# Performance work log

Hardware: AMD Instinct MI355X
Metric: run time of the kernel (lower is better)

The kernel has to match this reference:

```python
import jax, jax.numpy as jnp
import numpy as np


def setup_inputs() -> dict:
    key = jax.random.key(0)
    kx, kq, kb, kc = jax.random.split(key, 4)
    N, D = 16384, 1024
    x = jax.random.normal(kx, (N, D), dtype=jnp.float32)
    Q = jax.random.normal(kq, (D, D), dtype=jnp.float32)
    b = jax.random.normal(kb, (D,), dtype=jnp.float32)
    c = jax.random.normal(kc, (1,), dtype=jnp.float32)
    return {"x": x, "Q": Q, "b": b, "c": c}


def reference(x, Q, b, c):
    # y_i = x_i^T Q x_i + b^T x_i + c  (same math as diag(x @ Q @ x.T)
    # without materializing the NxN matrix)
    xQ = x @ Q                                # [N, D]
    quad = jnp.sum(xQ * x, axis=-1)           # [N]
    y = quad + x @ b + c                       # [N] (c broadcasts from [1])
    return y[:, None]                          # [N, 1]
```

## Files before the change

kernel.cpp:

```cpp
#include <hip/hip_runtime.h>
#include <hip/hip_bf16.h>


#define DD 1024
#define KH 256
#define KSTEP 8
#define NROUND 16
#define LDS_ROW 264

typedef short v8s __attribute__((ext_vector_type(8)));
typedef float v4f __attribute__((ext_vector_type(4)));

__device__ __forceinline__ short f2b(float f) {
    union { __hip_bfloat16 h; short s; } u;
    u.h = __float2bfloat16(f);
    return u.s;
}

__global__ __launch_bounds__(512, 2)
void quad_kernel(const float* __restrict__ x, const float* __restrict__ Q,
                 const float* __restrict__ bvec, const float* __restrict__ cptr,
                 float* __restrict__ y)
{
    __shared__ short lq[2][32 * LDS_ROW];

    const int tid  = threadIdx.x;
    const int lane = tid & 63;
    const int wave = tid >> 6;
    const int quad = lane >> 4;
    const int l15  = lane & 15;

    const int seg  = blockIdx.x & 7;
    const int rblk = blockIdx.x >> 3;
    const int kq   = seg >> 1;
    const int cs   = seg & 1;

    const int row_base = rblk * 256 + wave * 32;
    const int kofs     = kq * KH;
    const int col_base = cs * 512;

    v8s a[2][KSTEP];
    #pragma unroll
    for (int g = 0; g < 2; ++g) {
        const float* xr = x + (size_t)(row_base + g * 16 + l15) * DD + kofs + quad * 8;
        #pragma unroll
        for (int s = 0; s < KSTEP; ++s) {
            const float4 f0 = *(const float4*)(xr + s * 32);
            const float4 f1 = *(const float4*)(xr + s * 32 + 4);
            v8s t;
            t[0]=f2b(f0.x); t[1]=f2b(f0.y); t[2]=f2b(f0.z); t[3]=f2b(f0.w);
            t[4]=f2b(f1.x); t[5]=f2b(f1.y); t[6]=f2b(f1.z); t[7]=f2b(f1.w);
            a[g][s] = t;
            asm volatile("" : "+a"(a[g][s]));
        }
    }

    int s_nn[4], s_k4[4];
    #pragma unroll
    for (int i = 0; i < 4; ++i) {
        const int idx = tid + i * 512;
        s_nn[i] = idx >> 6;
        s_k4[i] = idx & 63;
    }

    float4 pf[4];
    #pragma unroll
    for (int i = 0; i < 4; ++i)
        pf[i] = *(const float4*)(Q + (size_t)(col_base + s_nn[i]) * DD + kofs + s_k4[i] * 4);

    float acc[2][4];
    #pragma unroll
    for (int g = 0; g < 2; ++g)
        #pragma unroll
        for (int r = 0; r < 4; ++r) acc[g][r] = 0.f;

    for (int t = 0; t < NROUND; ++t) {
        short* dst = &lq[t & 1][0];
        #pragma unroll
        for (int i = 0; i < 4; ++i) {
            const float4 f = pf[i];
            short4 s;
            s.x=f2b(f.x); s.y=f2b(f.y); s.z=f2b(f.z); s.w=f2b(f.w);
            *(short4*)&dst[s_nn[i] * LDS_ROW + s_k4[i] * 4] = s;
        }
        __syncthreads();

        if (t + 1 < NROUND) {
            #pragma unroll
            for (int i = 0; i < 4; ++i)
                pf[i] = *(const float4*)(Q + (size_t)(col_base + (t + 1) * 32 + s_nn[i]) * DD + kofs + s_k4[i] * 4);
        }

        const int n0 = col_base + t * 32 + l15;
        const float bn0 = (kq == 0) ? bvec[n0]      : 0.f;
        const float bn1 = (kq == 0) ? bvec[n0 + 16] : 0.f;
        float xv[2][2][4];
        {
            const float* xc = x + (size_t)(row_base + quad * 4) * DD + n0;
            #pragma unroll
            for (int nt = 0; nt < 2; ++nt)
                #pragma unroll
                for (int g = 0; g < 2; ++g)
                    #pragma unroll
                    for (int r = 0; r < 4; ++r)
                        xv[nt][g][r] = xc[(size_t)(g * 16 + r) * DD + nt * 16];
        }

        v4f cf[2][2];
        #pragma unroll
        for (int nt = 0; nt < 2; ++nt)
            #pragma unroll
            for (int g = 0; g < 2; ++g) cf[nt][g] = (v4f){0.f, 0.f, 0.f, 0.f};
        const short* bp = &lq[t & 1][l15 * LDS_ROW + quad * 8];
        #pragma unroll
        for (int s = 0; s < KSTEP; ++s) {
            const v8s b0 = *(const v8s*)(bp + s * 32);
            const v8s b1 = *(const v8s*)(bp + 16 * LDS_ROW + s * 32);
            #pragma unroll
            for (int g = 0; g < 2; ++g) {
                cf[0][g] = __builtin_amdgcn_mfma_f32_16x16x32_bf16(a[g][s], b0, cf[0][g], 0, 0, 0);
                cf[1][g] = __builtin_amdgcn_mfma_f32_16x16x32_bf16(a[g][s], b1, cf[1][g], 0, 0, 0);
            }
        }

        #pragma unroll
        for (int g = 0; g < 2; ++g)
            #pragma unroll
            for (int r = 0; r < 4; ++r)
                acc[g][r] += (cf[0][g][r] + bn0) * xv[0][g][r]
                           + (cf[1][g][r] + bn1) * xv[1][g][r];
    }

    const float cc = (seg == 0) ? cptr[0] : 0.f;
    #pragma unroll
    for (int g = 0; g < 2; ++g) {
        #pragma unroll
        for (int r = 0; r < 4; ++r) {
            float v = acc[g][r];
            v += __shfl_xor(v, 1); v += __shfl_xor(v, 2);
            v += __shfl_xor(v, 4); v += __shfl_xor(v, 8);
            if (l15 == 0)
                atomicAdd(&y[row_base + g * 16 + quad * 4 + r], v + cc);
        }
    }
}

extern "C" void kernel_launch(void* const* d_in, const int* in_sizes, int n_in,
                              void* d_out, int out_size, void* d_ws, size_t ws_size,
                              hipStream_t stream)
{
    const float* x = (const float*)d_in[0];
    const float* Q = (const float*)d_in[1];
    const float* b = (const float*)d_in[2];
    const float* c = (const float*)d_in[3];
    float* y = (float*)d_out;

    hipMemsetAsync(y, 0, (size_t)out_size * sizeof(float), stream);
    quad_kernel<<<dim3(512), dim3(512), 0, stream>>>(x, Q, b, c, y);
}
```

Baseline: 152.4 us.

## Stream Q tiles via global_load_lds with swizzled fp32 LDS and smaller K split

```diff
diff --git a/kernel.cpp b/kernel.cpp
--- a/kernel.cpp
+++ b/kernel.cpp
@@ -3,10 +3,11 @@
 
 
 #define DD 1024
-#define KH 256
-#define KSTEP 8
-#define NROUND 16
-#define LDS_ROW 264
+#define KH 128
+#define KSTEP 4
+#define NT 64
+#define ROWB 512
+#define TILEB 8192
 
 typedef short v8s __attribute__((ext_vector_type(8)));
 typedef float v4f __attribute__((ext_vector_type(4)));
@@ -17,12 +18,12 @@
     return u.s;
 }
 
-__global__ __launch_bounds__(512, 2)
+__global__ __launch_bounds__(256, 4)
 void quad_kernel(const float* __restrict__ x, const float* __restrict__ Q,
                  const float* __restrict__ bvec, const float* __restrict__ cptr,
                  float* __restrict__ y)
 {
-    __shared__ short lq[2][32 * LDS_ROW];
+    __shared__ __align__(1024) float lq[2][16 * KH];
 
     const int tid  = threadIdx.x;
     const int lane = tid & 63;
@@ -30,14 +31,28 @@
     const int quad = lane >> 4;
     const int l15  = lane & 15;
 
-    const int seg  = blockIdx.x & 7;
+    const int kq   = blockIdx.x & 7;
     const int rblk = blockIdx.x >> 3;
-    const int kq   = seg >> 1;
-    const int cs   = seg & 1;
+    const int row_base = rblk * 128 + wave * 32;
+    const int kofs = kq * KH;
 
-    const int row_base = rblk * 256 + wave * 32;
-    const int kofs     = kq * KH;
-    const int col_base = cs * 512;
+    int grow[2], goff[2];
+    #pragma unroll
+    for (int j = 0; j < 2; ++j) {
+        const int r = wave * 4 + j * 2 + (lane >> 5);
+        grow[j] = r;
+        goff[j] = ((lane & 31) * 16) ^ ((r & 7) << 4);
+    }
+
+    #pragma unroll
+    for (int j = 0; j < 2; ++j) {
+        const char* gp = (const char*)(Q + (size_t)grow[j] * DD + kofs) + goff[j];
+        __builtin_amdgcn_global_load_lds(
+            (const __attribute__((address_space(1))) unsigned int*)gp,
+            (__attribute__((address_space(3))) unsigned int*)
+                ((char*)&lq[0][0] + (wave * 4 + j * 2) * ROWB),
+            16, 0, 0);
+    }
 
     v8s a[2][KSTEP];
     #pragma unroll
@@ -55,18 +70,10 @@
         }
     }
 
-    int s_nn[4], s_k4[4];
-    #pragma unroll
-    for (int i = 0; i < 4; ++i) {
-        const int idx = tid + i * 512;
-        s_nn[i] = idx >> 6;
-        s_k4[i] = idx & 63;
-    }
-
-    float4 pf[4];
-    #pragma unroll
-    for (int i = 0; i < 4; ++i)
-        pf[i] = *(const float4*)(Q + (size_t)(col_base + s_nn[i]) * DD + kofs + s_k4[i] * 4);
+    const int xorc = (l15 & 7) << 4;
+    const int lp0 = l15 * ROWB + ((quad * 32     ) ^ xorc);
+    const int lp1 = l15 * ROWB + ((quad * 32 + 16) ^ xorc);
+    const char* lbase = (const char*)&lq[0][0];
 
     float acc[2][4];
     #pragma unroll
@@ -74,64 +81,56 @@
         #pragma unroll
         for (int r = 0; r < 4; ++r) acc[g][r] = 0.f;
 
-    for (int t = 0; t < NROUND; ++t) {
-        short* dst = &lq[t & 1][0];
-        #pragma unroll
-        for (int i = 0; i < 4; ++i) {
-            const float4 f = pf[i];
-            short4 s;
-            s.x=f2b(f.x); s.y=f2b(f.y); s.z=f2b(f.z); s.w=f2b(f.w);
-            *(short4*)&dst[s_nn[i] * LDS_ROW + s_k4[i] * 4] = s;
-        }
+    for (int t = 0; t < NT; ++t) {
         __syncthreads();
 
-        if (t + 1 < NROUND) {
+        if (t + 1 < NT) {
             #pragma unroll
-            for (int i = 0; i < 4; ++i)
-                pf[i] = *(const float4*)(Q + (size_t)(col_base + (t + 1) * 32 + s_nn[i]) * DD + kofs + s_k4[i] * 4);
+            for (int j = 0; j < 2; ++j) {
+                const char* gp = (const char*)(Q + (size_t)((t + 1) * 16 + grow[j]) * DD + kofs) + goff[j];
+                __builtin_amdgcn_global_load_lds(
+                    (const __attribute__((address_space(1))) unsigned int*)gp,
+                    (__attribute__((address_space(3))) unsigned int*)
+                        ((char*)&lq[(t + 1) & 1][0] + (wave * 4 + j * 2) * ROWB),
+                    16, 0, 0);
+            }
         }
 
-        const int n0 = col_base + t * 32 + l15;
-        const float bn0 = (kq == 0) ? bvec[n0]      : 0.f;
-        const float bn1 = (kq == 0) ? bvec[n0 + 16] : 0.f;
-        float xv[2][2][4];
+        const int n0 = t * 16 + l15;
+        const float bn = (kq == 0) ? bvec[n0] : 0.f;
+        float xv[2][4];
         {
             const float* xc = x + (size_t)(row_base + quad * 4) * DD + n0;
             #pragma unroll
-            for (int nt = 0; nt < 2; ++nt)
+            for (int g = 0; g < 2; ++g)
                 #pragma unroll
-                for (int g = 0; g < 2; ++g)
-                    #pragma unroll
-                    for (int r = 0; r < 4; ++r)
-                        xv[nt][g][r] = xc[(size_t)(g * 16 + r) * DD + nt * 16];
+                for (int r = 0; r < 4; ++r)
+                    xv[g][r] = xc[(size_t)(g * 16 + r) * DD];
         }
 
-        v4f cf[2][2];
-        #pragma unroll
-        for (int nt = 0; nt < 2; ++nt)
-            #pragma unroll
-            for (int g = 0; g < 2; ++g) cf[nt][g] = (v4f){0.f, 0.f, 0.f, 0.f};
-        const short* bp = &lq[t & 1][l15 * LDS_ROW + quad * 8];
+        const char* lb = lbase + (t & 1) * TILEB;
+        v4f cf[2];
+        cf[0] = (v4f){0.f, 0.f, 0.f, 0.f};
+        cf[1] = (v4f){0.f, 0.f, 0.f, 0.f};
         #pragma unroll
         for (int s = 0; s < KSTEP; ++s) {
-            const v8s b0 = *(const v8s*)(bp + s * 32);
-            const v8s b1 = *(const v8s*)(bp + 16 * LDS_ROW + s * 32);
-            #pragma unroll
-            for (int g = 0; g < 2; ++g) {
-                cf[0][g] = __builtin_amdgcn_mfma_f32_16x16x32_bf16(a[g][s], b0, cf[0][g], 0, 0, 0);
-                cf[1][g] = __builtin_amdgcn_mfma_f32_16x16x32_bf16(a[g][s], b1, cf[1][g], 0, 0, 0);
-            }
+            const float4 q0 = *(const float4*)(lb + lp0 + s * 128);
+            const float4 q1 = *(const float4*)(lb + lp1 + s * 128);
+            v8s bf;
+            bf[0]=f2b(q0.x); bf[1]=f2b(q0.y); bf[2]=f2b(q0.z); bf[3]=f2b(q0.w);
+            bf[4]=f2b(q1.x); bf[5]=f2b(q1.y); bf[6]=f2b(q1.z); bf[7]=f2b(q1.w);
+            cf[0] = __builtin_amdgcn_mfma_f32_16x16x32_bf16(a[0][s], bf, cf[0], 0, 0, 0);
+            cf[1] = __builtin_amdgcn_mfma_f32_16x16x32_bf16(a[1][s], bf, cf[1], 0, 0, 0);
         }
 
         #pragma unroll
         for (int g = 0; g < 2; ++g)
             #pragma unroll
             for (int r = 0; r < 4; ++r)
-                acc[g][r] += (cf[0][g][r] + bn0) * xv[0][g][r]
-                           + (cf[1][g][r] + bn1) * xv[1][g][r];
+                acc[g][r] += (cf[g][r] + bn) * xv[g][r];
     }
 
-    const float cc = (seg == 0) ? cptr[0] : 0.f;
+    const float cc = (kq == 0) ? cptr[0] : 0.f;
     #pragma unroll
     for (int g = 0; g < 2; ++g) {
         #pragma unroll
@@ -156,5 +155,5 @@
     float* y = (float*)d_out;
 
     hipMemsetAsync(y, 0, (size_t)out_size * sizeof(float), stream);
-    quad_kernel<<<dim3(512), dim3(512), 0, stream>>>(x, Q, b, c, y);
+    quad_kernel<<<dim3(1024), dim3(256), 0, stream>>>(x, Q, b, c, y);
 }
```

Result: slower. 177.2 us (+16.2%).
